# Optimization experiments

Measured on AMD Instinct MI355X. Metric: run time of the kernel, lower is better.

The kernel has to match this reference:

```python
import jax, jax.numpy as jnp
import numpy as np

B, T, I, H, O = 128, 512, 64, 1024, 12

def setup_inputs() -> dict:
    key = jax.random.key(0)
    ks = jax.random.split(key, 7)
    s_ih = 1.0 / np.sqrt(H)
    return {
        "x": jax.random.normal(ks[0], (B, T, I), dtype=jnp.float32),
        "W_ih": jax.random.normal(ks[1], (H, I), dtype=jnp.float32) * s_ih,
        "W_hh": jax.random.normal(ks[2], (H, H), dtype=jnp.float32) * s_ih,
        "b_ih": jax.random.normal(ks[3], (H,), dtype=jnp.float32) * s_ih,
        "b_hh": jax.random.normal(ks[4], (H,), dtype=jnp.float32) * s_ih,
        "W_out": jax.random.normal(ks[5], (O, H), dtype=jnp.float32) * s_ih,
        "b_out": jax.random.normal(ks[6], (O,), dtype=jnp.float32) * s_ih,
    }

def reference(x, W_ih, W_hh, b_ih, b_hh, W_out, b_out):
    # x: [B, T, I] (batch_first). Vanilla tanh RNN, h0 = 0.
    Bn, Tn, _ = x.shape
    Hn = W_hh.shape[0]
    # Precompute input projections for all timesteps (batched GEMM).
    xp = jnp.einsum('bti,hi->tbh', x, W_ih) + b_ih + b_hh  # [T, B, H]
    h0 = jnp.zeros((Bn, Hn), dtype=x.dtype)

    def step(h, xt):
        h_new = jnp.tanh(xt + h @ W_hh.T)
        return h_new, h_new

    _, hs = jax.lax.scan(step, h0, xp)  # hs: [T, B, H]
    hs = jnp.swapaxes(hs, 0, 1)         # [B, T, H]
    out = jnp.einsum('bth,oh->bto', hs, W_out) + b_out  # [B, T, O]
    return out.reshape(-1, 12)
```

## Files before the change

### kernel.cpp

```cpp
#include <hip/hip_runtime.h>
#include <hip/hip_bf16.h>

#define B_ 128
#define T_ 512
#define I_ 64
#define H_ 1024
#define O_ 12
#define HSTEP (H_ * B_)
#define XSTEP (I_ * B_)
#define RSLOT 16384
#define TIMEOUT 2000

typedef __attribute__((ext_vector_type(8))) short bf16x8;
typedef __attribute__((ext_vector_type(4))) float f32x4;

#define MFMA16 __builtin_amdgcn_mfma_f32_16x16x32_bf16

__device__ __forceinline__ float bf2f(unsigned short s) {
  unsigned u = ((unsigned)s) << 16; float f; __builtin_memcpy(&f, &u, 4); return f;
}
__device__ __forceinline__ unsigned short f2bf(float f) {
  unsigned u; __builtin_memcpy(&u, &f, 4);
  u += 0x7fffu + ((u >> 16) & 1u);
  return (unsigned short)(u >> 16);
}

__device__ __forceinline__ unsigned ldA32(const unsigned* p) {
  return __hip_atomic_load(p, __ATOMIC_RELAXED, __HIP_MEMORY_SCOPE_AGENT);
}
__device__ __forceinline__ void stA32(unsigned* p, unsigned v) {
  __hip_atomic_store(p, v, __ATOMIC_RELAXED, __HIP_MEMORY_SCOPE_AGENT);
}
__device__ __forceinline__ unsigned long long ldA64(const unsigned long long* p) {
  return __hip_atomic_load(p, __ATOMIC_RELAXED, __HIP_MEMORY_SCOPE_AGENT);
}

__device__ __forceinline__ void store32_sc0(unsigned* p, unsigned v) {
  asm volatile("global_store_dword %0, %1, off sc0" :: "v"(p), "v"(v) : "memory");
}
__device__ __forceinline__ unsigned poll_sc0(const unsigned* p) {
  unsigned v;
  asm volatile("global_load_dword %0, %1, off sc0\n\ts_waitcnt vmcnt(0)"
               : "=v"(v) : "v"(p) : "memory");
  return v;
}
__device__ __forceinline__ bf16x8 load16_sc0(const void* p) {
  bf16x8 v;
  asm volatile("global_load_dwordx4 %0, %1, off sc0" : "=v"(v) : "v"(p));
  return v;
}
__device__ __forceinline__ void waitv8(bf16x8& v0, bf16x8& v1, bf16x8& v2, bf16x8& v3,
                                       bf16x8& v4, bf16x8& v5, bf16x8& v6, bf16x8& v7) {
  asm volatile("s_waitcnt vmcnt(0)"
               : "+v"(v0), "+v"(v1), "+v"(v2), "+v"(v3),
                 "+v"(v4), "+v"(v5), "+v"(v6), "+v"(v7) :: "memory");
}

__global__ void prep_xp(const float* __restrict__ x,
                        unsigned short* __restrict__ xPhi) {
  const int t = blockIdx.x;
  for (int u = threadIdx.x; u < 1024; u += 256) {
    const int ib = u >> 7, b = u & 127;
    const float* src = x + ((size_t)b * T_ + t) * I_ + ib * 8;
    bf16x8 hi;
    #pragma unroll
    for (int j = 0; j < 8; ++j) hi[j] = (short)f2bf(src[j]);
    *(bf16x8*)(xPhi + ((size_t)t * 1024 + u) * 8) = hi;
  }
}

__global__ void prep_misc(const float* __restrict__ W_out, float* __restrict__ WoT,
                          unsigned* __restrict__ bar) {
  const int idx = blockIdx.x * 256 + threadIdx.x;
  if (idx < 1024) bar[idx] = 0u;
  const int k = idx >> 4, s = idx & 15;
  float v = 0.0f;
  if (s < 6)                 v = W_out[s * H_ + k];
  else if (s >= 8 && s < 14) v = W_out[(s - 2) * H_ + k];
  WoT[idx] = v;
}

__global__ __launch_bounds__(256, 1) void rnn_mfma(
    const float* __restrict__ W_ih, const float* __restrict__ W_hh,
    const float* __restrict__ b_ih, const float* __restrict__ b_hh,
    const unsigned short* __restrict__ xPhi, unsigned short* __restrict__ hP,
    unsigned short* __restrict__ rF, unsigned short* __restrict__ rS,
    unsigned* __restrict__ bar)
{
  __shared__ float part[4][544];
  __shared__ float biasS[32];
  __shared__ unsigned modeS;
  const int tid = threadIdx.x, bid = blockIdx.x;
  const int wave = tid >> 6, lane = tid & 63, quad = lane >> 4, ln = lane & 15;
  const int g = bid & 7, rg = bid >> 3;
  const int r0 = rg * 32, b0 = g * 16;
  if (tid < 32) biasS[tid] = b_ih[r0 + tid] + b_hh[r0 + tid];
  if (tid == 0) modeS = 1u;

  bf16x8 ahhi[2][8], ahlo[2][8];
  #pragma unroll
  for (int mt = 0; mt < 2; ++mt)
    #pragma unroll
    for (int kt = 0; kt < 8; ++kt) {
      const float* wp = W_hh + (size_t)(r0 + mt * 16 + ln) * H_
                        + wave * 256 + kt * 32 + quad * 8;
      #pragma unroll
      for (int j = 0; j < 8; ++j) {
        float v = wp[j];
        unsigned short h = f2bf(v);
        ahhi[mt][kt][j] = (short)h;
        ahlo[mt][kt][j] = (short)f2bf(v - bf2f(h));
      }
    }
  bf16x8 axhi[2], axlo[2];
  if (wave < 2)
    #pragma unroll
    for (int mt = 0; mt < 2; ++mt) {
      const float* wp = W_ih + (size_t)(r0 + mt * 16 + ln) * I_
                        + wave * 32 + quad * 8;
      #pragma unroll
      for (int j = 0; j < 8; ++j) {
        float v = wp[j];
        unsigned short h = f2bf(v);
        axhi[mt][j] = (short)h;
        axlo[mt][j] = (short)f2bf(v - bf2f(h));
      }
    }
  __syncthreads();
  unsigned mode = 1u;

  const int bcol = b0 + ln;
  unsigned short* rFg = rF + (size_t)g * 2 * RSLOT;
  unsigned short* rSg = rS + (size_t)g * 2 * RSLOT;

  f32x4 xacc0 = {0.f, 0.f, 0.f, 0.f}, xacc1 = {0.f, 0.f, 0.f, 0.f};
  auto computeX = [&](int t) {
    if (wave < 2) {
      const size_t xo = (((size_t)t * 8 + wave * 4 + quad) * B_ + bcol) * 8;
      bf16x8 bxh = *(const bf16x8*)(xPhi + xo);
      f32x4 t0 = {0.f, 0.f, 0.f, 0.f}, t1 = {0.f, 0.f, 0.f, 0.f};
      t0 = MFMA16(axhi[0], bxh, t0, 0, 0, 0);
      t0 = MFMA16(axlo[0], bxh, t0, 0, 0, 0);
      t1 = MFMA16(axhi[1], bxh, t1, 0, 0, 0);
      t1 = MFMA16(axlo[1], bxh, t1, 0, 0, 0);
      xacc0 = t0; xacc1 = t1;
    }
  };
  computeX(0);

  for (int t = 0; t < T_; ++t) {
    f32x4 accA0 = xacc0, accA1 = xacc1;
    f32x4 accB0 = {0.f, 0.f, 0.f, 0.f}, accB1 = {0.f, 0.f, 0.f, 0.f};

    if (t > 0) {
      const int soff = ((wave * 32 + quad) * 16 + ln) * 8;
      bf16x8 bh[8];
      if (mode) {
        const unsigned short* slot = rFg + ((t - 1) & 1) * RSLOT + soff;
        #pragma unroll
        for (int kt = 0; kt < 8; ++kt)
          bh[kt] = load16_sc0(slot + kt * 512);
        waitv8(bh[0], bh[1], bh[2], bh[3], bh[4], bh[5], bh[6], bh[7]);
      } else {
        const unsigned long long* slot =
            (const unsigned long long*)(rSg + ((t - 1) & 1) * RSLOT + soff);
        #pragma unroll
        for (int kt = 0; kt < 8; ++kt) {
          union { unsigned long long u[2]; bf16x8 v; } U;
          U.u[0] = ldA64(slot + kt * 128);
          U.u[1] = ldA64(slot + kt * 128 + 1);
          bh[kt] = U.v;
        }
      }
      #pragma unroll
      for (int kt = 0; kt < 8; ++kt) {
        accA0 = MFMA16(ahhi[0][kt], bh[kt], accA0, 0, 0, 0);
        accA1 = MFMA16(ahhi[1][kt], bh[kt], accA1, 0, 0, 0);
        accB0 = MFMA16(ahlo[0][kt], bh[kt], accB0, 0, 0, 0);
        accB1 = MFMA16(ahlo[1][kt], bh[kt], accB1, 0, 0, 0);
      }
    }

    #pragma unroll
    for (int r = 0; r < 4; ++r) {
      part[wave][r * 68 + lane]       = accA0[r] + accB0[r];
      part[wave][(4 + r) * 68 + lane] = accA1[r] + accB1[r];
    }
    __syncthreads();

    {
      const int n = tid & 15, rp = tid >> 4;
      const int m0 = rp * 2;
      unsigned short o[2];
      #pragma unroll
      for (int rr = 0; rr < 2; ++rr) {
        const int m = m0 + rr;
        const int f = ((m >> 4) * 4 + (m & 3)) * 68 + ((m >> 2) & 3) * 16 + n;
        float s = part[0][f] + part[1][f] + part[2][f] + part[3][f] + biasS[m];
        o[rr] = f2bf(tanhf(s));
      }
      const unsigned pk = (unsigned)o[0] | ((unsigned)o[1] << 16);
      const int R = r0 + m0;
      *(unsigned*)(hP + (size_t)t * HSTEP
                   + ((size_t)(R >> 3) * B_ + (b0 + n)) * 8 + (R & 7)) = pk;
      const int soff = ((R >> 3) * 16 + n) * 8 + (R & 7);
      store32_sc0((unsigned*)(rFg + (t & 1) * RSLOT + soff), pk);
      stA32      ((unsigned*)(rSg + (t & 1) * RSLOT + soff), pk);
    }

    if (t < T_ - 1) {
      computeX(t + 1);
      asm volatile("s_waitcnt vmcnt(0)" ::: "memory");
      __syncthreads();
      if (tid == 0) {
        store32_sc0(&bar[g * 32 + rg],      (unsigned)(t + 1));
        stA32      (&bar[256 + g * 32 + rg], (unsigned)(t + 1));
      }
      if (tid < 64) {
        int ok = 0;
        if (mode) {
          for (int it = 0; it < TIMEOUT && !ok; ++it) {
            unsigned v = (lane < 32) ? poll_sc0(&bar[g * 32 + lane]) : 0xffffffffu;
            ok = __all((int)(v >= (unsigned)(t + 1)));
          }
        }
        if (!ok) {
          if (tid == 0) modeS = 0u;
          for (;;) {
            unsigned v = (lane < 32) ? ldA32(&bar[256 + g * 32 + lane]) : 0xffffffffu;
            if (__all((int)(v >= (unsigned)(t + 1)))) break;
            __builtin_amdgcn_s_sleep(1);
          }
        }
      }
      __syncthreads();
      mode = modeS;
    }
  }
}

__global__ __launch_bounds__(256, 2) void out_proj(
    const unsigned short* __restrict__ hP, const float* __restrict__ WoT,
    const float* __restrict__ b_out, float* __restrict__ out)
{
  const int t = blockIdx.x;
  const int tid = threadIdx.x;
  const int b  = tid & 127;
  const int oh = tid >> 7;
  float a0 = b_out[oh * 6 + 0], a1 = b_out[oh * 6 + 1], a2 = b_out[oh * 6 + 2];
  float a3 = b_out[oh * 6 + 3], a4 = b_out[oh * 6 + 4], a5 = b_out[oh * 6 + 5];
  const unsigned short* hp = hP + (size_t)t * HSTEP + (size_t)b * 8;
  const float4* W4 = (const float4*)WoT;
  for (int kb = 0; kb < 128; ++kb) {
    bf16x8 hv = *(const bf16x8*)(hp + (size_t)kb * (B_ * 8));
    #pragma unroll
    for (int j = 0; j < 8; ++j) {
      const int k = kb * 8 + j;
      float h = bf2f((unsigned short)hv[j]);
      float4 wa = W4[k * 4 + oh * 2];
      float4 wb = W4[k * 4 + oh * 2 + 1];
      a0 += wa.x * h; a1 += wa.y * h; a2 += wa.z * h;
      a3 += wa.w * h; a4 += wb.x * h; a5 += wb.y * h;
    }
  }
  float* op = out + ((size_t)b * T_ + t) * O_ + oh * 6;
  op[0] = a0; op[1] = a1; op[2] = a2; op[3] = a3; op[4] = a4; op[5] = a5;
}

extern "C" void kernel_launch(void* const* d_in, const int* in_sizes, int n_in,
                              void* d_out, int out_size, void* d_ws, size_t ws_size,
                              hipStream_t stream)
{
  const float* x     = (const float*)d_in[0];
  const float* W_ih  = (const float*)d_in[1];
  const float* W_hh  = (const float*)d_in[2];
  const float* b_ih  = (const float*)d_in[3];
  const float* b_hh  = (const float*)d_in[4];
  const float* W_out = (const float*)d_in[5];
  const float* b_out = (const float*)d_in[6];
  float* out = (float*)d_out;

  unsigned short* hP   = (unsigned short*)d_ws;
  unsigned short* xPhi = hP + (size_t)T_ * HSTEP;
  float*          WoT  = (float*)(xPhi + (size_t)T_ * XSTEP);
  unsigned short* rF   = (unsigned short*)(WoT + (size_t)H_ * 16);
  unsigned short* rS   = rF + (size_t)8 * 2 * RSLOT;
  unsigned*       bar  = (unsigned*)(rS + (size_t)8 * 2 * RSLOT);

  prep_xp  <<<T_,  256, 0, stream>>>(x, xPhi);
  prep_misc<<<64,  256, 0, stream>>>(W_out, WoT, bar);
  rnn_mfma <<<256, 256, 0, stream>>>(W_ih, W_hh, b_ih, b_hh, xPhi, hP, rF, rS, bar);
  out_proj <<<T_,  256, 0, stream>>>(hP, WoT, b_out, out);
}
```

Baseline: 1.881 ms.

## Replace per-step barrier with sentinel-based data polling on hidden state

Measured after the change: 5.979 ms. 218% more time.

```diff
diff --git a/kernel.cpp b/kernel.cpp
--- a/kernel.cpp
+++ b/kernel.cpp
@@ -8,8 +8,8 @@
 #define O_ 12
 #define HSTEP (H_ * B_)
 #define XSTEP (I_ * B_)
-#define RSLOT 16384
 #define TIMEOUT 2000
+#define SENT 0x7FC07FC0u
 
 typedef __attribute__((ext_vector_type(8))) short bf16x8;
 typedef __attribute__((ext_vector_type(4))) float f32x4;
@@ -25,24 +25,15 @@
   return (unsigned short)(u >> 16);
 }
 
-__device__ __forceinline__ unsigned ldA32(const unsigned* p) {
+__device__ __forceinline__ unsigned long long ldA64(const unsigned long long* p) {
   return __hip_atomic_load(p, __ATOMIC_RELAXED, __HIP_MEMORY_SCOPE_AGENT);
 }
 __device__ __forceinline__ void stA32(unsigned* p, unsigned v) {
   __hip_atomic_store(p, v, __ATOMIC_RELAXED, __HIP_MEMORY_SCOPE_AGENT);
 }
-__device__ __forceinline__ unsigned long long ldA64(const unsigned long long* p) {
-  return __hip_atomic_load(p, __ATOMIC_RELAXED, __HIP_MEMORY_SCOPE_AGENT);
-}
 
 __device__ __forceinline__ void store32_sc0(unsigned* p, unsigned v) {
   asm volatile("global_store_dword %0, %1, off sc0" :: "v"(p), "v"(v) : "memory");
-}
-__device__ __forceinline__ unsigned poll_sc0(const unsigned* p) {
-  unsigned v;
-  asm volatile("global_load_dword %0, %1, off sc0\n\ts_waitcnt vmcnt(0)"
-               : "=v"(v) : "v"(p) : "memory");
-  return v;
 }
 __device__ __forceinline__ bf16x8 load16_sc0(const void* p) {
   bf16x8 v;
@@ -54,6 +45,15 @@
   asm volatile("s_waitcnt vmcnt(0)"
                : "+v"(v0), "+v"(v1), "+v"(v2), "+v"(v3),
                  "+v"(v4), "+v"(v5), "+v"(v6), "+v"(v7) :: "memory");
+}
+
+__global__ void prep_fill(unsigned short* __restrict__ hP) {
+  const size_t stride = (size_t)gridDim.x * 256 * 8;
+  size_t idx = ((size_t)blockIdx.x * 256 + threadIdx.x) * 8;
+  const short s = (short)0x7FC0;
+  bf16x8 v = {s, s, s, s, s, s, s, s};
+  const size_t total = (size_t)T_ * HSTEP;
+  for (; idx < total; idx += stride) *(bf16x8*)(hP + idx) = v;
 }
 
 __global__ void prep_xp(const float* __restrict__ x,
@@ -69,10 +69,8 @@
   }
 }
 
-__global__ void prep_misc(const float* __restrict__ W_out, float* __restrict__ WoT,
-                          unsigned* __restrict__ bar) {
+__global__ void prep_misc(const float* __restrict__ W_out, float* __restrict__ WoT) {
   const int idx = blockIdx.x * 256 + threadIdx.x;
-  if (idx < 1024) bar[idx] = 0u;
   const int k = idx >> 4, s = idx & 15;
   float v = 0.0f;
   if (s < 6)                 v = W_out[s * H_ + k];
@@ -83,19 +81,15 @@
 __global__ __launch_bounds__(256, 1) void rnn_mfma(
     const float* __restrict__ W_ih, const float* __restrict__ W_hh,
     const float* __restrict__ b_ih, const float* __restrict__ b_hh,
-    const unsigned short* __restrict__ xPhi, unsigned short* __restrict__ hP,
-    unsigned short* __restrict__ rF, unsigned short* __restrict__ rS,
-    unsigned* __restrict__ bar)
+    const unsigned short* __restrict__ xPhi, unsigned short* __restrict__ hP)
 {
-  __shared__ float part[4][544];
+  __shared__ float part[2][4][544];
   __shared__ float biasS[32];
-  __shared__ unsigned modeS;
   const int tid = threadIdx.x, bid = blockIdx.x;
   const int wave = tid >> 6, lane = tid & 63, quad = lane >> 4, ln = lane & 15;
   const int g = bid & 7, rg = bid >> 3;
   const int r0 = rg * 32, b0 = g * 16;
   if (tid < 32) biasS[tid] = b_ih[r0 + tid] + b_hh[r0 + tid];
-  if (tid == 0) modeS = 1u;
 
   bf16x8 ahhi[2][8], ahlo[2][8];
   #pragma unroll
@@ -127,11 +121,9 @@
       }
     }
   __syncthreads();
-  unsigned mode = 1u;
 
   const int bcol = b0 + ln;
-  unsigned short* rFg = rF + (size_t)g * 2 * RSLOT;
-  unsigned short* rSg = rS + (size_t)g * 2 * RSLOT;
+  const size_t cbase = ((size_t)(wave * 32 + quad) * B_ + bcol) * 8;
 
   f32x4 xacc0 = {0.f, 0.f, 0.f, 0.f}, xacc1 = {0.f, 0.f, 0.f, 0.f};
   auto computeX = [&](int t) {
@@ -147,29 +139,49 @@
     }
   };
   computeX(0);
+  bool slow = false;
 
   for (int t = 0; t < T_; ++t) {
     f32x4 accA0 = xacc0, accA1 = xacc1;
     f32x4 accB0 = {0.f, 0.f, 0.f, 0.f}, accB1 = {0.f, 0.f, 0.f, 0.f};
 
     if (t > 0) {
-      const int soff = ((wave * 32 + quad) * 16 + ln) * 8;
+      const unsigned short* pl = hP + (size_t)(t - 1) * HSTEP + cbase;
       bf16x8 bh[8];
-      if (mode) {
-        const unsigned short* slot = rFg + ((t - 1) & 1) * RSLOT + soff;
-        #pragma unroll
-        for (int kt = 0; kt < 8; ++kt)
-          bh[kt] = load16_sc0(slot + kt * 512);
-        waitv8(bh[0], bh[1], bh[2], bh[3], bh[4], bh[5], bh[6], bh[7]);
-      } else {
-        const unsigned long long* slot =
-            (const unsigned long long*)(rSg + ((t - 1) & 1) * RSLOT + soff);
+      if (!slow) {
+        unsigned need = 0xFFu;
+        int it = 0;
+        for (;;) {
+          #pragma unroll
+          for (int kt = 0; kt < 8; ++kt)
+            if (need & (1u << kt)) bh[kt] = load16_sc0(pl + kt * 4096);
+          waitv8(bh[0], bh[1], bh[2], bh[3], bh[4], bh[5], bh[6], bh[7]);
+          #pragma unroll
+          for (int kt = 0; kt < 8; ++kt)
+            if (need & (1u << kt)) {
+              union { bf16x8 v; unsigned u[4]; } U; U.v = bh[kt];
+              if (U.u[0] != SENT && U.u[1] != SENT &&
+                  U.u[2] != SENT && U.u[3] != SENT)
+                need &= ~(1u << kt);
+            }
+          if (__all(need == 0u)) break;
+          if (++it >= TIMEOUT) { slow = true; break; }
+        }
+      }
+      if (slow) {
         #pragma unroll
         for (int kt = 0; kt < 8; ++kt) {
-          union { unsigned long long u[2]; bf16x8 v; } U;
-          U.u[0] = ldA64(slot + kt * 128);
-          U.u[1] = ldA64(slot + kt * 128 + 1);
-          bh[kt] = U.v;
+          const unsigned long long* q = (const unsigned long long*)(pl + kt * 4096);
+          for (;;) {
+            union { unsigned long long u[2]; bf16x8 v; } U;
+            U.u[0] = ldA64(q); U.u[1] = ldA64(q + 1);
+            const unsigned w0 = (unsigned)U.u[0], w1 = (unsigned)(U.u[0] >> 32);
+            const unsigned w2 = (unsigned)U.u[1], w3 = (unsigned)(U.u[1] >> 32);
+            if (w0 != SENT && w1 != SENT && w2 != SENT && w3 != SENT) {
+              bh[kt] = U.v; break;
+            }
+            __builtin_amdgcn_s_sleep(1);
+          }
         }
       }
       #pragma unroll
@@ -183,8 +195,8 @@
 
     #pragma unroll
     for (int r = 0; r < 4; ++r) {
-      part[wave][r * 68 + lane]       = accA0[r] + accB0[r];
-      part[wave][(4 + r) * 68 + lane] = accA1[r] + accB1[r];
+      part[t & 1][wave][r * 68 + lane]       = accA0[r] + accB0[r];
+      part[t & 1][wave][(4 + r) * 68 + lane] = accA1[r] + accB1[r];
     }
     __syncthreads();
 
@@ -196,46 +208,19 @@
       for (int rr = 0; rr < 2; ++rr) {
         const int m = m0 + rr;
         const int f = ((m >> 4) * 4 + (m & 3)) * 68 + ((m >> 2) & 3) * 16 + n;
-        float s = part[0][f] + part[1][f] + part[2][f] + part[3][f] + biasS[m];
+        float s = part[t & 1][0][f] + part[t & 1][1][f]
+                + part[t & 1][2][f] + part[t & 1][3][f] + biasS[m];
         o[rr] = f2bf(tanhf(s));
       }
       const unsigned pk = (unsigned)o[0] | ((unsigned)o[1] << 16);
       const int R = r0 + m0;
-      *(unsigned*)(hP + (size_t)t * HSTEP
-                   + ((size_t)(R >> 3) * B_ + (b0 + n)) * 8 + (R & 7)) = pk;
-      const int soff = ((R >> 3) * 16 + n) * 8 + (R & 7);
-      store32_sc0((unsigned*)(rFg + (t & 1) * RSLOT + soff), pk);
-      stA32      ((unsigned*)(rSg + (t & 1) * RSLOT + soff), pk);
-    }
-
-    if (t < T_ - 1) {
-      computeX(t + 1);
-      asm volatile("s_waitcnt vmcnt(0)" ::: "memory");
-      __syncthreads();
-      if (tid == 0) {
-        store32_sc0(&bar[g * 32 + rg],      (unsigned)(t + 1));
-        stA32      (&bar[256 + g * 32 + rg], (unsigned)(t + 1));
-      }
-      if (tid < 64) {
-        int ok = 0;
-        if (mode) {
-          for (int it = 0; it < TIMEOUT && !ok; ++it) {
-            unsigned v = (lane < 32) ? poll_sc0(&bar[g * 32 + lane]) : 0xffffffffu;
-            ok = __all((int)(v >= (unsigned)(t + 1)));
-          }
-        }
-        if (!ok) {
-          if (tid == 0) modeS = 0u;
-          for (;;) {
-            unsigned v = (lane < 32) ? ldA32(&bar[256 + g * 32 + lane]) : 0xffffffffu;
-            if (__all((int)(v >= (unsigned)(t + 1)))) break;
-            __builtin_amdgcn_s_sleep(1);
-          }
-        }
-      }
-      __syncthreads();
-      mode = modeS;
-    }
+      unsigned* dst = (unsigned*)(hP + (size_t)t * HSTEP
+                      + ((size_t)(R >> 3) * B_ + (b0 + n)) * 8 + (R & 7));
+      store32_sc0(dst, pk);
+      stA32(dst, pk);
+    }
+
+    if (t < T_ - 1) computeX(t + 1);
   }
 }
 
@@ -283,12 +268,10 @@
   unsigned short* hP   = (unsigned short*)d_ws;
   unsigned short* xPhi = hP + (size_t)T_ * HSTEP;
   float*          WoT  = (float*)(xPhi + (size_t)T_ * XSTEP);
-  unsigned short* rF   = (unsigned short*)(WoT + (size_t)H_ * 16);
-  unsigned short* rS   = rF + (size_t)8 * 2 * RSLOT;
-  unsigned*       bar  = (unsigned*)(rS + (size_t)8 * 2 * RSLOT);
-
-  prep_xp  <<<T_,  256, 0, stream>>>(x, xPhi);
-  prep_misc<<<64,  256, 0, stream>>>(W_out, WoT, bar);
-  rnn_mfma <<<256, 256, 0, stream>>>(W_ih, W_hh, b_ih, b_hh, xPhi, hP, rF, rS, bar);
-  out_proj <<<T_,  256, 0, stream>>>(hP, WoT, b_out, out);
-}
+
+  prep_fill<<<2048, 256, 0, stream>>>(hP);
+  prep_xp  <<<T_,   256, 0, stream>>>(x, xPhi);
+  prep_misc<<<64,   256, 0, stream>>>(W_out, WoT);
+  rnn_mfma <<<256,  256, 0, stream>>>(W_ih, W_hh, b_ih, b_hh, xPhi, hP);
+  out_proj <<<T_,   256, 0, stream>>>(hP, WoT, b_out, out);
+}
```

## Replace fallback barrier with NaN-sentinel polling on hP and trim per-step sync

Applied to the files above, without the earlier changes.

Measured after the change: 2.713 ms. 1.44x slower.

```diff
diff --git a/kernel.cpp b/kernel.cpp
--- a/kernel.cpp
+++ b/kernel.cpp
@@ -10,6 +10,7 @@
 #define XSTEP (I_ * B_)
 #define RSLOT 16384
 #define TIMEOUT 2000
+#define SENT 0x7FC07FC0u
 
 typedef __attribute__((ext_vector_type(8))) short bf16x8;
 typedef __attribute__((ext_vector_type(4))) float f32x4;
@@ -25,14 +26,11 @@
   return (unsigned short)(u >> 16);
 }
 
-__device__ __forceinline__ unsigned ldA32(const unsigned* p) {
+__device__ __forceinline__ unsigned long long ldA64(const unsigned long long* p) {
   return __hip_atomic_load(p, __ATOMIC_RELAXED, __HIP_MEMORY_SCOPE_AGENT);
 }
 __device__ __forceinline__ void stA32(unsigned* p, unsigned v) {
   __hip_atomic_store(p, v, __ATOMIC_RELAXED, __HIP_MEMORY_SCOPE_AGENT);
-}
-__device__ __forceinline__ unsigned long long ldA64(const unsigned long long* p) {
-  return __hip_atomic_load(p, __ATOMIC_RELAXED, __HIP_MEMORY_SCOPE_AGENT);
 }
 
 __device__ __forceinline__ void store32_sc0(unsigned* p, unsigned v) {
@@ -54,6 +52,15 @@
   asm volatile("s_waitcnt vmcnt(0)"
                : "+v"(v0), "+v"(v1), "+v"(v2), "+v"(v3),
                  "+v"(v4), "+v"(v5), "+v"(v6), "+v"(v7) :: "memory");
+}
+
+__global__ void prep_fill(unsigned short* __restrict__ hP) {
+  const size_t stride = (size_t)gridDim.x * 256 * 8;
+  size_t idx = ((size_t)blockIdx.x * 256 + threadIdx.x) * 8;
+  const short s = (short)0x7FC0;
+  bf16x8 v = {s, s, s, s, s, s, s, s};
+  const size_t total = (size_t)T_ * HSTEP;
+  for (; idx < total; idx += stride) *(bf16x8*)(hP + idx) = v;
 }
 
 __global__ void prep_xp(const float* __restrict__ x,
@@ -84,11 +91,11 @@
     const float* __restrict__ W_ih, const float* __restrict__ W_hh,
     const float* __restrict__ b_ih, const float* __restrict__ b_hh,
     const unsigned short* __restrict__ xPhi, unsigned short* __restrict__ hP,
-    unsigned short* __restrict__ rF, unsigned short* __restrict__ rS,
-    unsigned* __restrict__ bar)
+    unsigned short* __restrict__ rF, unsigned* __restrict__ bar)
 {
   __shared__ float part[4][544];
   __shared__ float biasS[32];
+  __shared__ unsigned pkS[256];
   __shared__ unsigned modeS;
   const int tid = threadIdx.x, bid = blockIdx.x;
   const int wave = tid >> 6, lane = tid & 63, quad = lane >> 4, ln = lane & 15;
@@ -131,7 +138,7 @@
 
   const int bcol = b0 + ln;
   unsigned short* rFg = rF + (size_t)g * 2 * RSLOT;
-  unsigned short* rSg = rS + (size_t)g * 2 * RSLOT;
+  const size_t cbase = ((size_t)(wave * 32 + quad) * B_ + bcol) * 8;
 
   f32x4 xacc0 = {0.f, 0.f, 0.f, 0.f}, xacc1 = {0.f, 0.f, 0.f, 0.f};
   auto computeX = [&](int t) {
@@ -153,23 +160,29 @@
     f32x4 accB0 = {0.f, 0.f, 0.f, 0.f}, accB1 = {0.f, 0.f, 0.f, 0.f};
 
     if (t > 0) {
-      const int soff = ((wave * 32 + quad) * 16 + ln) * 8;
       bf16x8 bh[8];
       if (mode) {
+        const int soff = ((wave * 32 + quad) * 16 + ln) * 8;
         const unsigned short* slot = rFg + ((t - 1) & 1) * RSLOT + soff;
         #pragma unroll
         for (int kt = 0; kt < 8; ++kt)
           bh[kt] = load16_sc0(slot + kt * 512);
         waitv8(bh[0], bh[1], bh[2], bh[3], bh[4], bh[5], bh[6], bh[7]);
       } else {
-        const unsigned long long* slot =
-            (const unsigned long long*)(rSg + ((t - 1) & 1) * RSLOT + soff);
+        const unsigned short* pl = hP + (size_t)(t - 1) * HSTEP + cbase;
         #pragma unroll
         for (int kt = 0; kt < 8; ++kt) {
-          union { unsigned long long u[2]; bf16x8 v; } U;
-          U.u[0] = ldA64(slot + kt * 128);
-          U.u[1] = ldA64(slot + kt * 128 + 1);
-          bh[kt] = U.v;
+          const unsigned long long* q = (const unsigned long long*)(pl + kt * 4096);
+          for (;;) {
+            union { unsigned long long u[2]; bf16x8 v; } U;
+            U.u[0] = ldA64(q); U.u[1] = ldA64(q + 1);
+            const unsigned w0 = (unsigned)U.u[0], w1 = (unsigned)(U.u[0] >> 32);
+            const unsigned w2 = (unsigned)U.u[1], w3 = (unsigned)(U.u[1] >> 32);
+            if (w0 != SENT && w1 != SENT && w2 != SENT && w3 != SENT) {
+              bh[kt] = U.v; break;
+            }
+            __builtin_amdgcn_s_sleep(1);
+          }
         }
       }
       #pragma unroll
@@ -188,6 +201,7 @@
     }
     __syncthreads();
 
+    unsigned pk; unsigned* hPdst;
     {
       const int n = tid & 15, rp = tid >> 4;
       const int m0 = rp * 2;
@@ -199,39 +213,40 @@
         float s = part[0][f] + part[1][f] + part[2][f] + part[3][f] + biasS[m];
         o[rr] = f2bf(tanhf(s));
       }
-      const unsigned pk = (unsigned)o[0] | ((unsigned)o[1] << 16);
+      pk = (unsigned)o[0] | ((unsigned)o[1] << 16);
       const int R = r0 + m0;
-      *(unsigned*)(hP + (size_t)t * HSTEP
-                   + ((size_t)(R >> 3) * B_ + (b0 + n)) * 8 + (R & 7)) = pk;
-      const int soff = ((R >> 3) * 16 + n) * 8 + (R & 7);
-      store32_sc0((unsigned*)(rFg + (t & 1) * RSLOT + soff), pk);
-      stA32      ((unsigned*)(rSg + (t & 1) * RSLOT + soff), pk);
+      hPdst = (unsigned*)(hP + (size_t)t * HSTEP
+                          + ((size_t)(R >> 3) * B_ + (b0 + n)) * 8 + (R & 7));
+      store32_sc0((unsigned*)(rFg + (t & 1) * RSLOT
+                              + ((R >> 3) * 16 + n) * 8 + (R & 7)), pk);
+      store32_sc0(hPdst, pk);
+      pkS[tid] = pk;
     }
 
     if (t < T_ - 1) {
-      computeX(t + 1);
       asm volatile("s_waitcnt vmcnt(0)" ::: "memory");
       __syncthreads();
-      if (tid == 0) {
-        store32_sc0(&bar[g * 32 + rg],      (unsigned)(t + 1));
-        stA32      (&bar[256 + g * 32 + rg], (unsigned)(t + 1));
-      }
-      if (tid < 64) {
+      if (tid == 0) store32_sc0(&bar[g * 32 + rg], (unsigned)(t + 1));
+
+      if (wave == 2) {
+        const int p = tid + 64;
+        const int pn = p & 15, pm0 = (p >> 4) * 2;
+        const int PR = r0 + pm0;
+        unsigned* pdst = (unsigned*)(hP + (size_t)t * HSTEP
+                         + ((size_t)(PR >> 3) * B_ + (b0 + pn)) * 8 + (PR & 7));
+        stA32(pdst, pkS[p]);
+      }
+      if (wave < 3) stA32(hPdst, pk);
+
+      computeX(t + 1);
+
+      if (wave == 3 && mode) {
         int ok = 0;
-        if (mode) {
-          for (int it = 0; it < TIMEOUT && !ok; ++it) {
-            unsigned v = (lane < 32) ? poll_sc0(&bar[g * 32 + lane]) : 0xffffffffu;
-            ok = __all((int)(v >= (unsigned)(t + 1)));
-          }
+        for (int it = 0; it < TIMEOUT && !ok; ++it) {
+          unsigned v = (lane < 32) ? poll_sc0(&bar[g * 32 + lane]) : 0xffffffffu;
+          ok = __all((int)(v >= (unsigned)(t + 1)));
         }
-        if (!ok) {
-          if (tid == 0) modeS = 0u;
-          for (;;) {
-            unsigned v = (lane < 32) ? ldA32(&bar[256 + g * 32 + lane]) : 0xffffffffu;
-            if (__all((int)(v >= (unsigned)(t + 1)))) break;
-            __builtin_amdgcn_s_sleep(1);
-          }
-        }
+        if (!ok && lane == 0) modeS = 0u;
       }
       __syncthreads();
       mode = modeS;
@@ -284,11 +299,11 @@
   unsigned short* xPhi = hP + (size_t)T_ * HSTEP;
   float*          WoT  = (float*)(xPhi + (size_t)T_ * XSTEP);
   unsigned short* rF   = (unsigned short*)(WoT + (size_t)H_ * 16);
-  unsigned short* rS   = rF + (size_t)8 * 2 * RSLOT;
-  unsigned*       bar  = (unsigned*)(rS + (size_t)8 * 2 * RSLOT);
-
-  prep_xp  <<<T_,  256, 0, stream>>>(x, xPhi);
-  prep_misc<<<64,  256, 0, stream>>>(W_out, WoT, bar);
-  rnn_mfma <<<256, 256, 0, stream>>>(W_ih, W_hh, b_ih, b_hh, xPhi, hP, rF, rS, bar);
-  out_proj <<<T_,  256, 0, stream>>>(hP, WoT, b_out, out);
-}
+  unsigned*       bar  = (unsigned*)(rF + (size_t)8 * 2 * RSLOT);
+
+  prep_fill<<<2048, 256, 0, stream>>>(hP);
+  prep_xp  <<<T_,   256, 0, stream>>>(x, xPhi);
+  prep_misc<<<64,   256, 0, stream>>>(W_out, WoT, bar);
+  rnn_mfma <<<256,  256, 0, stream>>>(W_ih, W_hh, b_ih, b_hh, xPhi, hP, rF, bar);
+  out_proj <<<T_,   256, 0, stream>>>(hP, WoT, b_out, out);
+}
```

## Fuse output projection into recurrent kernel via per-step partial sums and atomics

Applied to the files above, without the earlier changes.

After: 1.786 ms. -5.1%, faster.

```diff
diff --git a/kernel.cpp b/kernel.cpp
--- a/kernel.cpp
+++ b/kernel.cpp
@@ -6,7 +6,6 @@
 #define I_ 64
 #define H_ 1024
 #define O_ 12
-#define HSTEP (H_ * B_)
 #define XSTEP (I_ * B_)
 #define RSLOT 16384
 #define TIMEOUT 2000
@@ -69,25 +68,28 @@
   }
 }
 
-__global__ void prep_misc(const float* __restrict__ W_out, float* __restrict__ WoT,
+__global__ void prep_misc(const float* __restrict__ b_out, float* __restrict__ out,
                           unsigned* __restrict__ bar) {
   const int idx = blockIdx.x * 256 + threadIdx.x;
   if (idx < 1024) bar[idx] = 0u;
-  const int k = idx >> 4, s = idx & 15;
-  float v = 0.0f;
-  if (s < 6)                 v = W_out[s * H_ + k];
-  else if (s >= 8 && s < 14) v = W_out[(s - 2) * H_ + k];
-  WoT[idx] = v;
+  float bo[12];
+  #pragma unroll
+  for (int o = 0; o < 12; ++o) bo[o] = b_out[o];
+  for (int r = idx; r < B_ * T_; r += 16384) {
+    #pragma unroll
+    for (int o = 0; o < 12; ++o) out[(size_t)r * 12 + o] = bo[o];
+  }
 }
 
 __global__ __launch_bounds__(256, 1) void rnn_mfma(
     const float* __restrict__ W_ih, const float* __restrict__ W_hh,
     const float* __restrict__ b_ih, const float* __restrict__ b_hh,
-    const unsigned short* __restrict__ xPhi, unsigned short* __restrict__ hP,
+    const float* __restrict__ W_out, const unsigned short* __restrict__ xPhi,
     unsigned short* __restrict__ rF, unsigned short* __restrict__ rS,
-    unsigned* __restrict__ bar)
+    unsigned* __restrict__ bar, float* __restrict__ out)
 {
   __shared__ float part[4][544];
+  __shared__ float outS[16 * 16 * 12];
   __shared__ float biasS[32];
   __shared__ unsigned modeS;
   const int tid = threadIdx.x, bid = blockIdx.x;
@@ -96,6 +98,16 @@
   const int r0 = rg * 32, b0 = g * 16;
   if (tid < 32) biasS[tid] = b_ih[r0 + tid] + b_hh[r0 + tid];
   if (tid == 0) modeS = 1u;
+
+  float wo[12][2];
+  {
+    const int R = r0 + (tid >> 4) * 2;
+    #pragma unroll
+    for (int o = 0; o < 12; ++o) {
+      wo[o][0] = W_out[(size_t)o * H_ + R];
+      wo[o][1] = W_out[(size_t)o * H_ + R + 1];
+    }
+  }
 
   bf16x8 ahhi[2][8], ahlo[2][8];
   #pragma unroll
@@ -147,6 +159,17 @@
     }
   };
   computeX(0);
+
+  auto outReduce = [&](int t) {
+    if (tid >= 64) {
+      const int j = tid - 64;
+      const int n2 = j / 12, o = j - n2 * 12;
+      float acc = 0.f;
+      #pragma unroll
+      for (int rp2 = 0; rp2 < 16; ++rp2) acc += outS[(n2 * 16 + rp2) * 12 + o];
+      atomicAdd(&out[((size_t)(b0 + n2) * T_ + t) * 12 + o], acc);
+    }
+  };
 
   for (int t = 0; t < T_; ++t) {
     f32x4 accA0 = xacc0, accA1 = xacc1;
@@ -191,21 +214,24 @@
     {
       const int n = tid & 15, rp = tid >> 4;
       const int m0 = rp * 2;
-      unsigned short o[2];
+      float hv[2];
+      unsigned short o2[2];
       #pragma unroll
       for (int rr = 0; rr < 2; ++rr) {
         const int m = m0 + rr;
         const int f = ((m >> 4) * 4 + (m & 3)) * 68 + ((m >> 2) & 3) * 16 + n;
         float s = part[0][f] + part[1][f] + part[2][f] + part[3][f] + biasS[m];
-        o[rr] = f2bf(tanhf(s));
-      }
-      const unsigned pk = (unsigned)o[0] | ((unsigned)o[1] << 16);
+        hv[rr] = tanhf(s);
+        o2[rr] = f2bf(hv[rr]);
+      }
+      const unsigned pk = (unsigned)o2[0] | ((unsigned)o2[1] << 16);
       const int R = r0 + m0;
-      *(unsigned*)(hP + (size_t)t * HSTEP
-                   + ((size_t)(R >> 3) * B_ + (b0 + n)) * 8 + (R & 7)) = pk;
       const int soff = ((R >> 3) * 16 + n) * 8 + (R & 7);
       store32_sc0((unsigned*)(rFg + (t & 1) * RSLOT + soff), pk);
       stA32      ((unsigned*)(rSg + (t & 1) * RSLOT + soff), pk);
+      #pragma unroll
+      for (int o = 0; o < 12; ++o)
+        outS[(n * 16 + rp) * 12 + o] = wo[o][0] * hv[0] + wo[o][1] * hv[1];
     }
 
     if (t < T_ - 1) {
@@ -232,39 +258,16 @@
             __builtin_amdgcn_s_sleep(1);
           }
         }
+      } else {
+        outReduce(t);
       }
       __syncthreads();
       mode = modeS;
     }
   }
-}
-
-__global__ __launch_bounds__(256, 2) void out_proj(
-    const unsigned short* __restrict__ hP, const float* __restrict__ WoT,
-    const float* __restrict__ b_out, float* __restrict__ out)
-{
-  const int t = blockIdx.x;
-  const int tid = threadIdx.x;
-  const int b  = tid & 127;
-  const int oh = tid >> 7;
-  float a0 = b_out[oh * 6 + 0], a1 = b_out[oh * 6 + 1], a2 = b_out[oh * 6 + 2];
-  float a3 = b_out[oh * 6 + 3], a4 = b_out[oh * 6 + 4], a5 = b_out[oh * 6 + 5];
-  const unsigned short* hp = hP + (size_t)t * HSTEP + (size_t)b * 8;
-  const float4* W4 = (const float4*)WoT;
-  for (int kb = 0; kb < 128; ++kb) {
-    bf16x8 hv = *(const bf16x8*)(hp + (size_t)kb * (B_ * 8));
-    #pragma unroll
-    for (int j = 0; j < 8; ++j) {
-      const int k = kb * 8 + j;
-      float h = bf2f((unsigned short)hv[j]);
-      float4 wa = W4[k * 4 + oh * 2];
-      float4 wb = W4[k * 4 + oh * 2 + 1];
-      a0 += wa.x * h; a1 += wa.y * h; a2 += wa.z * h;
-      a3 += wa.w * h; a4 += wb.x * h; a5 += wb.y * h;
-    }
-  }
-  float* op = out + ((size_t)b * T_ + t) * O_ + oh * 6;
-  op[0] = a0; op[1] = a1; op[2] = a2; op[3] = a3; op[4] = a4; op[5] = a5;
+
+  __syncthreads();
+  outReduce(T_ - 1);
 }
 
 extern "C" void kernel_launch(void* const* d_in, const int* in_sizes, int n_in,
@@ -280,15 +283,13 @@
   const float* b_out = (const float*)d_in[6];
   float* out = (float*)d_out;
 
-  unsigned short* hP   = (unsigned short*)d_ws;
-  unsigned short* xPhi = hP + (size_t)T_ * HSTEP;
-  float*          WoT  = (float*)(xPhi + (size_t)T_ * XSTEP);
-  unsigned short* rF   = (unsigned short*)(WoT + (size_t)H_ * 16);
+  unsigned short* xPhi = (unsigned short*)d_ws;
+  unsigned short* rF   = xPhi + (size_t)T_ * XSTEP;
   unsigned short* rS   = rF + (size_t)8 * 2 * RSLOT;
   unsigned*       bar  = (unsigned*)(rS + (size_t)8 * 2 * RSLOT);
 
   prep_xp  <<<T_,  256, 0, stream>>>(x, xPhi);
-  prep_misc<<<64,  256, 0, stream>>>(W_out, WoT, bar);
-  rnn_mfma <<<256, 256, 0, stream>>>(W_ih, W_hh, b_ih, b_hh, xPhi, hP, rF, rS, bar);
-  out_proj <<<T_,  256, 0, stream>>>(hP, WoT, b_out, out);
-}
+  prep_misc<<<64,  256, 0, stream>>>(b_out, out, bar);
+  rnn_mfma <<<256, 256, 0, stream>>>(W_ih, W_hh, b_ih, b_hh, W_out,
+                                     xPhi, rF, rS, bar, out);
+}
```
